# Optimization experiments

Hardware: AMD Instinct MI355X
Metric: run time of the kernel (lower is better)

Reference implementation:

```python
import jax, jax.numpy as jnp
import numpy as np

B = 16384
INPUT_DIM = 256
NUM_SLOTS = 32
SLOT_DIM = 64
NUM_KNOWN = 9
HIDDEN = 128
ITERS = 3
LN_EPS = 1e-5


def _lin(k, fan_in, w_shape, b_shape):
    # torch nn.Linear default init: U(-1/sqrt(fan_in), 1/sqrt(fan_in))
    bound = 1.0 / np.sqrt(fan_in)
    k1, k2 = jax.random.split(k)
    W = jax.random.uniform(k1, w_shape, jnp.float32, -bound, bound)
    b = jax.random.uniform(k2, b_shape, jnp.float32, -bound, bound)
    return W, b


def setup_inputs() -> dict:
    key = jax.random.key(0)
    ks = jax.random.split(key, 20)
    inp = {}
    inp['world_state'] = jax.random.normal(ks[0], (B, INPUT_DIM), jnp.float32)
    inp['eps'] = jax.random.normal(ks[1], (B, NUM_SLOTS, SLOT_DIM), jnp.float32)
    inp['slots_mu'] = jax.random.normal(ks[2], (1, NUM_SLOTS, SLOT_DIM), jnp.float32)
    inp['slots_sigma'] = jnp.ones((1, NUM_SLOTS, SLOT_DIM), jnp.float32) * 0.1
    inp['Wi'], inp['bi'] = _lin(ks[3], INPUT_DIM, (INPUT_DIM, SLOT_DIM), (SLOT_DIM,))
    inp['Wk'], inp['bk'] = _lin(ks[4], SLOT_DIM, (SLOT_DIM, SLOT_DIM), (SLOT_DIM,))
    inp['Wq'], inp['bq'] = _lin(ks[5], SLOT_DIM, (SLOT_DIM, SLOT_DIM), (SLOT_DIM,))
    inp['Wv'], inp['bv'] = _lin(ks[6], SLOT_DIM, (SLOT_DIM, SLOT_DIM), (SLOT_DIM,))
    inp['W_ih'], inp['b_ih'] = _lin(ks[7], SLOT_DIM, (SLOT_DIM, 3 * SLOT_DIM), (3 * SLOT_DIM,))
    inp['W_hh'], inp['b_hh'] = _lin(ks[8], SLOT_DIM, (SLOT_DIM, 3 * SLOT_DIM), (3 * SLOT_DIM,))
    inp['W1'], inp['b1'] = _lin(ks[9], SLOT_DIM, (SLOT_DIM, HIDDEN), (HIDDEN,))
    inp['W2'], inp['b2'] = _lin(ks[10], HIDDEN, (HIDDEN, SLOT_DIM), (SLOT_DIM,))
    inp['g_in'] = jnp.ones((SLOT_DIM,), jnp.float32)
    inp['b_in'] = jnp.zeros((SLOT_DIM,), jnp.float32)
    inp['g_sl'] = jnp.ones((SLOT_DIM,), jnp.float32)
    inp['b_sl'] = jnp.zeros((SLOT_DIM,), jnp.float32)
    inp['g_mlp'] = jnp.ones((SLOT_DIM,), jnp.float32)
    inp['b_mlp'] = jnp.zeros((SLOT_DIM,), jnp.float32)
    inp['Wh1'], inp['bh1'] = _lin(ks[11], SLOT_DIM, (NUM_KNOWN, SLOT_DIM, SLOT_DIM // 2), (NUM_KNOWN, SLOT_DIM // 2))
    inp['Wh2'], inp['bh2'] = _lin(ks[12], SLOT_DIM // 2, (NUM_KNOWN, SLOT_DIM // 2), (NUM_KNOWN,))
    return inp


def _ln(x, g, b):
    mu = jnp.mean(x, axis=-1, keepdims=True)
    var = jnp.mean(jnp.square(x - mu), axis=-1, keepdims=True)
    return (x - mu) / jnp.sqrt(var + LN_EPS) * g + b


def reference(world_state, eps, slots_mu, slots_sigma, Wi, bi, Wk, bk, Wq, bq, Wv, bv,
              W_ih, b_ih, W_hh, b_hh, W1, b1, W2, b2,
              g_in, b_in, g_sl, b_sl, g_mlp, b_mlp, Wh1, bh1, Wh2, bh2):
    scale = SLOT_DIM ** (-0.5)
    x = world_state[:, None, :] @ Wi + bi            # [B,1,D]
    x = _ln(x, g_in, b_in)
    k = x @ Wk + bk                                   # [B,1,D] (loop-invariant)
    v = x @ Wv + bv                                   # [B,1,D]
    slots = slots_mu + slots_sigma * eps              # [B,S,D]
    for _ in range(ITERS):
        prev = slots
        sn = _ln(slots, g_sl, b_sl)
        q = sn @ Wq + bq                              # [B,S,D]
        attn = jnp.einsum('bnd,bsd->bns', k, q) * scale  # [B,1,S]
        attn = jax.nn.softmax(attn, axis=-1) + 1e-8
        attn = attn / jnp.sum(attn, axis=1, keepdims=True)  # dual normalization
        upd = jnp.einsum('bns,bnd->bsd', attn, v)     # [B,S,D]
        # GRUCell
        gi = upd @ W_ih + b_ih                        # [B,S,3D]
        gh = prev @ W_hh + b_hh
        r = jax.nn.sigmoid(gi[..., :SLOT_DIM] + gh[..., :SLOT_DIM])
        z = jax.nn.sigmoid(gi[..., SLOT_DIM:2 * SLOT_DIM] + gh[..., SLOT_DIM:2 * SLOT_DIM])
        n = jnp.tanh(gi[..., 2 * SLOT_DIM:] + r * gh[..., 2 * SLOT_DIM:])
        slots = (1.0 - z) * n + z * prev
        # residual MLP
        h = _ln(slots, g_mlp, b_mlp)
        slots = slots + jax.nn.gelu(h @ W1 + b1, approximate=False) @ W2 + b2
    # known property heads (vectorized over 9 heads)
    s9 = slots[:, :NUM_KNOWN, :]                      # [B,9,D]
    hh = jax.nn.gelu(jnp.einsum('bkd,kdh->bkh', s9, Wh1) + bh1, approximate=False)
    pv = jax.nn.sigmoid(jnp.einsum('bkh,kh->bk', hh, Wh2) + bh2)  # [B,9]
    free_act = jnp.sqrt(jnp.sum(jnp.square(slots[:, NUM_KNOWN:, :]), axis=-1)).mean(axis=0)  # [num_free]
    return (pv, slots, free_act)
```

## Files before the change

kernel.cpp:

```cpp
#include <hip/hip_runtime.h>


typedef __attribute__((ext_vector_type(4))) float f32x4;
typedef __attribute__((ext_vector_type(8))) short s16x8;

#define MFMA16 __builtin_amdgcn_mfma_f32_16x16x32_bf16

#define NB       16384
#define GIB_OFF  (32 + 120*256)
#define PV_N     147456
#define SLOT_N   33554432
#define L2E      1.4426950408889634f

__device__ __forceinline__ unsigned short f2bf(float f){
  unsigned int r;
  asm("v_cvt_pk_bf16_f32 %0, %1, 0" : "=v"(r) : "v"(f));
  return (unsigned short)r;
}
__device__ __forceinline__ float bf2f(unsigned short s){
  unsigned int u = ((unsigned int)s) << 16;
  return __builtin_bit_cast(float, u);
}
__device__ __forceinline__ float sigm(float x){
  return __builtin_amdgcn_rcpf(1.f + __expf(-x));
}
__device__ __forceinline__ float sigm2(float y){
  return __builtin_amdgcn_rcpf(1.f + exp2f(-y));
}
__device__ __forceinline__ float tanh2(float y){
  return 1.f - 2.f*__builtin_amdgcn_rcpf(1.f + exp2f(y));
}
__device__ __forceinline__ float geluf(float x){
  float t = x*x;
  float p = __builtin_fmaf(t, 0.044715f, 1.f);
  float y = (x*2.3022090f)*p;
  return x * __builtin_amdgcn_rcpf(1.f + exp2f(-y));
}

__global__ void prep1_pack(const float* __restrict__ Wi, const float* __restrict__ Wv,
                           const float* __restrict__ Wih, const float* __restrict__ Whh,
                           const float* __restrict__ W1, const float* __restrict__ W2,
                           float* __restrict__ wsf){
  int t = blockIdx.x*256 + threadIdx.x;
  if (blockIdx.x == 0 && threadIdx.x < 32) wsf[threadIdx.x] = 0.f;
  if (t >= 120*64) return;
  int frag = t >> 6, lane = t & 63;
  int q = lane >> 4, idx = lane & 15;
  const float* W; int ncols, ct, kf;
  if      (frag < 24){ W=Whh; ncols=192; ct=frag>>1;      kf=frag&1; }
  else if (frag < 40){ int f=frag-24; W=W1;  ncols=128; ct=f>>1; kf=f&1; }
  else if (frag < 56){ int f=frag-40; W=W2;  ncols=64;  ct=f>>2; kf=f&3; }
  else if (frag < 88){ int f=frag-56; W=Wi;  ncols=64;  ct=f>>3; kf=f&7; }
  else if (frag < 96){ int f=frag-88; W=Wv;  ncols=64;  ct=f>>1; kf=f&1; }
  else               { int f=frag-96; W=Wih; ncols=192; ct=f>>1; kf=f&1; }
  int k0 = kf*32 + q*8;
  int n  = ct*16 + idx;
  float sc = 1.f;
  if (frag < 24) sc = (n < 128) ? L2E : 2.f*L2E;
  unsigned short* dst = (unsigned short*)(wsf + 32) + frag*512 + lane*8;
  #pragma unroll
  for (int j = 0; j < 8; ++j) dst[j] = f2bf(W[(size_t)(k0+j)*ncols + n] * sc);
}

__global__ __launch_bounds__(256) void prep2_gi(
    const float* __restrict__ wstate, const float* __restrict__ bi,
    const float* __restrict__ bv, const float* __restrict__ bih,
    const float* __restrict__ g_in, const float* __restrict__ b_in,
    float* __restrict__ wsf){
  __shared__ __align__(16) unsigned short sxn[4][1152];
  const f32x4 zf = {0.f,0.f,0.f,0.f};
  int tid = threadIdx.x;
  int w = __builtin_amdgcn_readfirstlane(tid >> 6);
  int lane = tid & 63, q = lane >> 4, idx = lane & 15;
  int br0 = blockIdx.x*64 + w*16;
  const unsigned short* fb = (const unsigned short*)(wsf + 32);
  float* gib = wsf + GIB_OFF;

  s16x8 af[8];
  #pragma unroll
  for (int kf = 0; kf < 8; ++kf){
    const float* src = wstate + (size_t)(br0+idx)*256 + kf*32 + q*8;
    f32x4 p0 = *(const f32x4*)(src);
    f32x4 p1 = *(const f32x4*)(src+4);
    s16x8 a;
    a[0]=(short)f2bf(p0[0]); a[1]=(short)f2bf(p0[1]); a[2]=(short)f2bf(p0[2]); a[3]=(short)f2bf(p0[3]);
    a[4]=(short)f2bf(p1[0]); a[5]=(short)f2bf(p1[1]); a[6]=(short)f2bf(p1[2]); a[7]=(short)f2bf(p1[3]);
    af[kf] = a;
  }
  float xv[4][4];
  #pragma unroll
  for (int ct = 0; ct < 4; ++ct){
    f32x4 acc = zf;
    #pragma unroll
    for (int kf = 0; kf < 8; ++kf)
      acc = MFMA16(af[kf], *(const s16x8*)(fb + (56 + ct*8 + kf)*512 + lane*8), acc, 0,0,0);
    float bb = bi[ct*16+idx];
    #pragma unroll
    for (int e = 0; e < 4; ++e) xv[ct][e] = acc[e] + bb;
  }
  #pragma unroll
  for (int e = 0; e < 4; ++e){
    float s1 = xv[0][e]+xv[1][e]+xv[2][e]+xv[3][e];
    float s2 = xv[0][e]*xv[0][e]+xv[1][e]*xv[1][e]+xv[2][e]*xv[2][e]+xv[3][e]*xv[3][e];
    #pragma unroll
    for (int m = 1; m < 16; m <<= 1){ s1 += __shfl_xor(s1,m); s2 += __shfl_xor(s2,m); }
    float mean = s1*(1.f/64.f);
    float var  = s2*(1.f/64.f) - mean*mean;
    float rs   = __builtin_amdgcn_rsqf(var + 1e-5f);
    #pragma unroll
    for (int ct = 0; ct < 4; ++ct){
      int c = ct*16+idx;
      sxn[w][(q*4+e)*72 + c] = f2bf((xv[ct][e]-mean)*rs*g_in[c] + b_in[c]);
    }
  }
  s16x8 xa0 = *(const s16x8*)(&sxn[w][idx*72 + q*8]);
  s16x8 xa1 = *(const s16x8*)(&sxn[w][idx*72 + 32 + q*8]);
  #pragma unroll
  for (int ct = 0; ct < 4; ++ct){
    f32x4 acc = MFMA16(xa0, *(const s16x8*)(fb + (88 + ct*2 + 0)*512 + lane*8), zf, 0,0,0);
    acc       = MFMA16(xa1, *(const s16x8*)(fb + (88 + ct*2 + 1)*512 + lane*8), acc, 0,0,0);
    float bb = bv[ct*16+idx];
    #pragma unroll
    for (int e = 0; e < 4; ++e) sxn[w][(q*4+e)*72 + ct*16+idx] = f2bf(acc[e] + bb);
  }
  s16x8 va0 = *(const s16x8*)(&sxn[w][idx*72 + q*8]);
  s16x8 va1 = *(const s16x8*)(&sxn[w][idx*72 + 32 + q*8]);
  #pragma unroll
  for (int ct = 0; ct < 12; ++ct){
    f32x4 acc = MFMA16(va0, *(const s16x8*)(fb + (96 + ct*2 + 0)*512 + lane*8), zf, 0,0,0);
    acc       = MFMA16(va1, *(const s16x8*)(fb + (96 + ct*2 + 1)*512 + lane*8), acc, 0,0,0);
    float bb = bih[ct*16+idx];
    float sc = (ct < 8) ? L2E : 2.f*L2E;
    #pragma unroll
    for (int e = 0; e < 4; ++e)
      gib[(size_t)(br0 + q*4 + e)*192 + ct*16 + idx] = (acc[e] + bb) * sc;
  }
}

__global__ __launch_bounds__(512, 4) void bank_main(
    const float* __restrict__ eps, const float* __restrict__ smu, const float* __restrict__ ssig,
    const float* __restrict__ bhh, const float* __restrict__ b1v, const float* __restrict__ b2v,
    const float* __restrict__ g_mlp, const float* __restrict__ b_mlp,
    const float* __restrict__ Wh1, const float* __restrict__ bh1,
    const float* __restrict__ Wh2, const float* __restrict__ bh2,
    float* __restrict__ wsf, float* __restrict__ out){
  __shared__ __align__(16) unsigned short swgt[20480];
  __shared__ __align__(16) unsigned short sbuf[8][2176];
  __shared__ float sgi[4][192];
  __shared__ float sbias[512];
  __shared__ float sfree[4][24];
  const f32x4 zf = {0.f,0.f,0.f,0.f};
  int tid = threadIdx.x;
  int w = __builtin_amdgcn_readfirstlane(tid >> 6);
  int lane = tid & 63, q = lane >> 4, idx = lane & 15;
  int pair = w >> 1, half = w & 1;
  int b = blockIdx.x*4 + pair;
  const unsigned short* fb = (const unsigned short*)(wsf + 32);
  const float* gib = wsf + GIB_OFF;

  {
    const uint4* src = (const uint4*)fb;
    uint4* dst = (uint4*)swgt;
    #pragma unroll
    for (int i = 0; i < 5; ++i) dst[tid + 512*i] = src[tid + 512*i];
  }
  {
    int i = tid;
    float vv;
    if      (i < 192) vv = bhh[i] * ((i < 128) ? L2E : 2.f*L2E);
    else if (i < 320) vv = b1v[i-192];
    else if (i < 384) vv = b2v[i-320];
    else if (i < 448) vv = g_mlp[i-384];
    else              vv = b_mlp[i-448];
    sbias[i] = vv;
  }
  if (half == 0){
    #pragma unroll
    for (int jj = 0; jj < 3; ++jj) sgi[pair][jj*64+lane] = gib[(size_t)b*192 + jj*64 + lane];
  }
  unsigned short* S = &sbuf[w][0];
  int s0 = half*16;
  #pragma unroll
  for (int rr = 0; rr < 16; ++rr){
    int s = s0 + rr;
    float ev = eps[((size_t)b*32 + s)*64 + lane];
    S[rr*136 + lane] = f2bf(smu[s*64+lane] + ssig[s*64+lane]*ev);
  }
  __syncthreads();

  size_t obase = (size_t)PV_N + ((size_t)b*32 + s0)*64;
  #pragma unroll 1
  for (int it = 0; it < 3; ++it){
    s16x8 a0 = *(const s16x8*)(&S[idx*136 + q*8]);
    s16x8 a1 = *(const s16x8*)(&S[idx*136 + 32 + q*8]);
    f32x4 gacc[12];
    #pragma unroll
    for (int ct = 0; ct < 12; ++ct){
      f32x4 acc = MFMA16(a0, *(const s16x8*)(&swgt[(ct*2+0)*512 + lane*8]), zf, 0,0,0);
      gacc[ct]  = MFMA16(a1, *(const s16x8*)(&swgt[(ct*2+1)*512 + lane*8]), acc, 0,0,0);
    }
    float nsv[4][4];
    #pragma unroll
    for (int ct = 0; ct < 4; ++ct){
      int c = ct*16+idx;
      float cr = sgi[pair][c]     + sbias[c];
      float cz = sgi[pair][64+c]  + sbias[64+c];
      float cn = sgi[pair][128+c];
      float bn = sbias[128+c];
      #pragma unroll
      for (int e = 0; e < 4; ++e){
        float r = sigm2(cr + gacc[ct][e]);
        float z = sigm2(cz + gacc[4+ct][e]);
        float n = tanh2(cn + r*(gacc[8+ct][e] + bn));
        float prev = bf2f(S[(q*4+e)*136 + c]);
        nsv[ct][e] = (1.f - z)*n + z*prev;
      }
    }
    #pragma unroll
    for (int e = 0; e < 4; ++e){
      float s1 = nsv[0][e]+nsv[1][e]+nsv[2][e]+nsv[3][e];
      float s2 = nsv[0][e]*nsv[0][e]+nsv[1][e]*nsv[1][e]+nsv[2][e]*nsv[2][e]+nsv[3][e]*nsv[3][e];
      #pragma unroll
      for (int m = 1; m < 16; m <<= 1){ s1 += __shfl_xor(s1,m); s2 += __shfl_xor(s2,m); }
      float mean = s1*(1.f/64.f);
      float var  = s2*(1.f/64.f) - mean*mean;
      float rs   = __builtin_amdgcn_rsqf(var + 1e-5f);
      #pragma unroll
      for (int ct = 0; ct < 4; ++ct){
        int c = ct*16+idx;
        S[(q*4+e)*136 + c] = f2bf((nsv[ct][e]-mean)*rs*sbias[384+c] + sbias[448+c]);
      }
    }
    s16x8 h0 = *(const s16x8*)(&S[idx*136 + q*8]);
    s16x8 h1 = *(const s16x8*)(&S[idx*136 + 32 + q*8]);
    f32x4 macc[8];
    #pragma unroll
    for (int ct = 0; ct < 8; ++ct){
      f32x4 acc = MFMA16(h0, *(const s16x8*)(&swgt[(24+ct*2+0)*512 + lane*8]), zf, 0,0,0);
      macc[ct]  = MFMA16(h1, *(const s16x8*)(&swgt[(24+ct*2+1)*512 + lane*8]), acc, 0,0,0);
    }
    #pragma unroll
    for (int ct = 0; ct < 8; ++ct){
      int c = ct*16+idx;
      float bb = sbias[192+c];
      #pragma unroll
      for (int e = 0; e < 4; ++e)
        S[(q*4+e)*136 + c] = f2bf(geluf(macc[ct][e] + bb));
    }
    s16x8 t0 = *(const s16x8*)(&S[idx*136 +       q*8]);
    s16x8 t1 = *(const s16x8*)(&S[idx*136 + 32  + q*8]);
    s16x8 t2 = *(const s16x8*)(&S[idx*136 + 64  + q*8]);
    s16x8 t3 = *(const s16x8*)(&S[idx*136 + 96  + q*8]);
    #pragma unroll
    for (int ct = 0; ct < 4; ++ct){
      f32x4 acc = MFMA16(t0, *(const s16x8*)(fb + (40+ct*4+0)*512 + lane*8), zf, 0,0,0);
      acc       = MFMA16(t1, *(const s16x8*)(fb + (40+ct*4+1)*512 + lane*8), acc, 0,0,0);
      acc       = MFMA16(t2, *(const s16x8*)(fb + (40+ct*4+2)*512 + lane*8), acc, 0,0,0);
      acc       = MFMA16(t3, *(const s16x8*)(fb + (40+ct*4+3)*512 + lane*8), acc, 0,0,0);
      int c = ct*16+idx;
      float bb = sbias[320+c];
      #pragma unroll
      for (int e = 0; e < 4; ++e){
        float val = nsv[ct][e] + acc[e] + bb;
        S[(q*4+e)*136 + c] = f2bf(val);
        if (it == 2) out[obase + (size_t)(q*4+e)*64 + c] = val;
      }
    }
  }
  __syncthreads();

  if (half == 0){
    int hh = lane & 31, h2 = lane >> 5;
    #pragma unroll 1
    for (int kb = 0; kb < 5; ++kb){
      int k = kb*2 + h2;
      if (k < 9){
        const float* wp = Wh1 + (size_t)k*2048 + hh;
        float a0=0.f, a1=0.f, a2=0.f, a3=0.f;
        #pragma unroll 4
        for (int dd = 0; dd < 64; dd += 4){
          a0 += bf2f(S[k*136 + dd  ]) * wp[(dd  )*32];
          a1 += bf2f(S[k*136 + dd+1]) * wp[(dd+1)*32];
          a2 += bf2f(S[k*136 + dd+2]) * wp[(dd+2)*32];
          a3 += bf2f(S[k*136 + dd+3]) * wp[(dd+3)*32];
        }
        float a = bh1[k*32 + hh] + (a0 + a1) + (a2 + a3);
        float u = geluf(a);
        float p = u * Wh2[k*32 + hh];
        #pragma unroll
        for (int m = 1; m < 32; m <<= 1) p += __shfl_xor(p, m);
        p = sigm(p + bh2[k]);
        if (hh == 0) out[(size_t)b*9 + k] = p;
      }
    }
  } else {
    const unsigned short* SL = &sbuf[w-1][0];
    #pragma unroll 1
    for (int s = 9; s < 32; ++s){
      const unsigned short* src = (s < 16) ? (SL + s*136) : (S + (s-16)*136);
      float v = bf2f(src[lane]);
      float sq = v*v;
      #pragma unroll
      for (int m = 1; m < 64; m <<= 1) sq += __shfl_xor(sq, m);
      if (lane == 0) sfree[pair][s-9] = sqrtf(sq);
    }
  }
  __syncthreads();
  if (tid < 23) atomicAdd(&wsf[tid], sfree[0][tid] + sfree[1][tid] + sfree[2][tid] + sfree[3][tid]);
}

__global__ void bank_final(const float* __restrict__ wsf, float* __restrict__ out){
  int t = threadIdx.x;
  if (t < 23) out[(size_t)PV_N + SLOT_N + t] = wsf[t] * (1.f/16384.f);
}

extern "C" void kernel_launch(void* const* d_in, const int* in_sizes, int n_in,
                              void* d_out, int out_size, void* d_ws, size_t ws_size,
                              hipStream_t stream){
  (void)in_sizes; (void)n_in; (void)out_size; (void)ws_size;
  const float* wstate = (const float*)d_in[0];
  const float* eps    = (const float*)d_in[1];
  const float* smu    = (const float*)d_in[2];
  const float* ssig   = (const float*)d_in[3];
  const float* Wi     = (const float*)d_in[4];
  const float* bi     = (const float*)d_in[5];
  const float* Wv     = (const float*)d_in[10];
  const float* bv     = (const float*)d_in[11];
  const float* Wih    = (const float*)d_in[12];
  const float* bih    = (const float*)d_in[13];
  const float* Whh    = (const float*)d_in[14];
  const float* bhh    = (const float*)d_in[15];
  const float* W1     = (const float*)d_in[16];
  const float* b1     = (const float*)d_in[17];
  const float* W2     = (const float*)d_in[18];
  const float* b2     = (const float*)d_in[19];
  const float* g_in   = (const float*)d_in[20];
  const float* b_in   = (const float*)d_in[21];
  const float* g_mlp  = (const float*)d_in[24];
  const float* b_mlp  = (const float*)d_in[25];
  const float* Wh1    = (const float*)d_in[26];
  const float* bh1    = (const float*)d_in[27];
  const float* Wh2    = (const float*)d_in[28];
  const float* bh2    = (const float*)d_in[29];
  float* out = (float*)d_out;
  float* wsf = (float*)d_ws;

  prep1_pack<<<dim3(30),   dim3(256), 0, stream>>>(Wi, Wv, Wih, Whh, W1, W2, wsf);
  prep2_gi  <<<dim3(256),  dim3(256), 0, stream>>>(wstate, bi, bv, bih, g_in, b_in, wsf);
  bank_main <<<dim3(4096), dim3(512), 0, stream>>>(eps, smu, ssig, bhh, b1, b2,
                                                   g_mlp, b_mlp, Wh1, bh1, Wh2, bh2,
                                                   wsf, out);
  bank_final<<<dim3(1),    dim3(64),  0, stream>>>(wsf, out);
}
```

Baseline: 637.0 us.

## Fuse input projection into main kernel and read weights from global/L1

```diff
diff --git a/kernel.cpp b/kernel.cpp
--- a/kernel.cpp
+++ b/kernel.cpp
@@ -7,15 +7,14 @@
 #define MFMA16 __builtin_amdgcn_mfma_f32_16x16x32_bf16
 
 #define NB       16384
-#define GIB_OFF  (32 + 120*256)
 #define PV_N     147456
 #define SLOT_N   33554432
 #define L2E      1.4426950408889634f
 
 __device__ __forceinline__ unsigned short f2bf(float f){
-  unsigned int r;
-  asm("v_cvt_pk_bf16_f32 %0, %1, 0" : "=v"(r) : "v"(f));
-  return (unsigned short)r;
+  unsigned int u = __builtin_bit_cast(unsigned int, f);
+  u += 0x7fffu + ((u >> 16) & 1u);
+  return (unsigned short)(u >> 16);
 }
 __device__ __forceinline__ float bf2f(unsigned short s){
   unsigned int u = ((unsigned int)s) << 16;
@@ -62,90 +61,18 @@
   for (int j = 0; j < 8; ++j) dst[j] = f2bf(W[(size_t)(k0+j)*ncols + n] * sc);
 }
 
-__global__ __launch_bounds__(256) void prep2_gi(
-    const float* __restrict__ wstate, const float* __restrict__ bi,
-    const float* __restrict__ bv, const float* __restrict__ bih,
+__global__ __launch_bounds__(512, 6) void bank_main(
+    const float* __restrict__ wstate,
+    const float* __restrict__ eps, const float* __restrict__ smu, const float* __restrict__ ssig,
+    const float* __restrict__ bi, const float* __restrict__ bv, const float* __restrict__ bih,
     const float* __restrict__ g_in, const float* __restrict__ b_in,
-    float* __restrict__ wsf){
-  __shared__ __align__(16) unsigned short sxn[4][1152];
-  const f32x4 zf = {0.f,0.f,0.f,0.f};
-  int tid = threadIdx.x;
-  int w = __builtin_amdgcn_readfirstlane(tid >> 6);
-  int lane = tid & 63, q = lane >> 4, idx = lane & 15;
-  int br0 = blockIdx.x*64 + w*16;
-  const unsigned short* fb = (const unsigned short*)(wsf + 32);
-  float* gib = wsf + GIB_OFF;
-
-  s16x8 af[8];
-  #pragma unroll
-  for (int kf = 0; kf < 8; ++kf){
-    const float* src = wstate + (size_t)(br0+idx)*256 + kf*32 + q*8;
-    f32x4 p0 = *(const f32x4*)(src);
-    f32x4 p1 = *(const f32x4*)(src+4);
-    s16x8 a;
-    a[0]=(short)f2bf(p0[0]); a[1]=(short)f2bf(p0[1]); a[2]=(short)f2bf(p0[2]); a[3]=(short)f2bf(p0[3]);
-    a[4]=(short)f2bf(p1[0]); a[5]=(short)f2bf(p1[1]); a[6]=(short)f2bf(p1[2]); a[7]=(short)f2bf(p1[3]);
-    af[kf] = a;
-  }
-  float xv[4][4];
-  #pragma unroll
-  for (int ct = 0; ct < 4; ++ct){
-    f32x4 acc = zf;
-    #pragma unroll
-    for (int kf = 0; kf < 8; ++kf)
-      acc = MFMA16(af[kf], *(const s16x8*)(fb + (56 + ct*8 + kf)*512 + lane*8), acc, 0,0,0);
-    float bb = bi[ct*16+idx];
-    #pragma unroll
-    for (int e = 0; e < 4; ++e) xv[ct][e] = acc[e] + bb;
-  }
-  #pragma unroll
-  for (int e = 0; e < 4; ++e){
-    float s1 = xv[0][e]+xv[1][e]+xv[2][e]+xv[3][e];
-    float s2 = xv[0][e]*xv[0][e]+xv[1][e]*xv[1][e]+xv[2][e]*xv[2][e]+xv[3][e]*xv[3][e];
-    #pragma unroll
-    for (int m = 1; m < 16; m <<= 1){ s1 += __shfl_xor(s1,m); s2 += __shfl_xor(s2,m); }
-    float mean = s1*(1.f/64.f);
-    float var  = s2*(1.f/64.f) - mean*mean;
-    float rs   = __builtin_amdgcn_rsqf(var + 1e-5f);
-    #pragma unroll
-    for (int ct = 0; ct < 4; ++ct){
-      int c = ct*16+idx;
-      sxn[w][(q*4+e)*72 + c] = f2bf((xv[ct][e]-mean)*rs*g_in[c] + b_in[c]);
-    }
-  }
-  s16x8 xa0 = *(const s16x8*)(&sxn[w][idx*72 + q*8]);
-  s16x8 xa1 = *(const s16x8*)(&sxn[w][idx*72 + 32 + q*8]);
-  #pragma unroll
-  for (int ct = 0; ct < 4; ++ct){
-    f32x4 acc = MFMA16(xa0, *(const s16x8*)(fb + (88 + ct*2 + 0)*512 + lane*8), zf, 0,0,0);
-    acc       = MFMA16(xa1, *(const s16x8*)(fb + (88 + ct*2 + 1)*512 + lane*8), acc, 0,0,0);
-    float bb = bv[ct*16+idx];
-    #pragma unroll
-    for (int e = 0; e < 4; ++e) sxn[w][(q*4+e)*72 + ct*16+idx] = f2bf(acc[e] + bb);
-  }
-  s16x8 va0 = *(const s16x8*)(&sxn[w][idx*72 + q*8]);
-  s16x8 va1 = *(const s16x8*)(&sxn[w][idx*72 + 32 + q*8]);
-  #pragma unroll
-  for (int ct = 0; ct < 12; ++ct){
-    f32x4 acc = MFMA16(va0, *(const s16x8*)(fb + (96 + ct*2 + 0)*512 + lane*8), zf, 0,0,0);
-    acc       = MFMA16(va1, *(const s16x8*)(fb + (96 + ct*2 + 1)*512 + lane*8), acc, 0,0,0);
-    float bb = bih[ct*16+idx];
-    float sc = (ct < 8) ? L2E : 2.f*L2E;
-    #pragma unroll
-    for (int e = 0; e < 4; ++e)
-      gib[(size_t)(br0 + q*4 + e)*192 + ct*16 + idx] = (acc[e] + bb) * sc;
-  }
-}
-
-__global__ __launch_bounds__(512, 4) void bank_main(
-    const float* __restrict__ eps, const float* __restrict__ smu, const float* __restrict__ ssig,
     const float* __restrict__ bhh, const float* __restrict__ b1v, const float* __restrict__ b2v,
     const float* __restrict__ g_mlp, const float* __restrict__ b_mlp,
     const float* __restrict__ Wh1, const float* __restrict__ bh1,
     const float* __restrict__ Wh2, const float* __restrict__ bh2,
     float* __restrict__ wsf, float* __restrict__ out){
-  __shared__ __align__(16) unsigned short swgt[20480];
   __shared__ __align__(16) unsigned short sbuf[8][2176];
+  __shared__ __align__(16) unsigned short sxn[1152];
   __shared__ float sgi[4][192];
   __shared__ float sbias[512];
   __shared__ float sfree[4][24];
@@ -156,14 +83,7 @@
   int pair = w >> 1, half = w & 1;
   int b = blockIdx.x*4 + pair;
   const unsigned short* fb = (const unsigned short*)(wsf + 32);
-  const float* gib = wsf + GIB_OFF;
-
-  {
-    const uint4* src = (const uint4*)fb;
-    uint4* dst = (uint4*)swgt;
-    #pragma unroll
-    for (int i = 0; i < 5; ++i) dst[tid + 512*i] = src[tid + 512*i];
-  }
+
   {
     int i = tid;
     float vv;
@@ -174,10 +94,6 @@
     else              vv = b_mlp[i-448];
     sbias[i] = vv;
   }
-  if (half == 0){
-    #pragma unroll
-    for (int jj = 0; jj < 3; ++jj) sgi[pair][jj*64+lane] = gib[(size_t)b*192 + jj*64 + lane];
-  }
   unsigned short* S = &sbuf[w][0];
   int s0 = half*16;
   #pragma unroll
@@ -186,6 +102,70 @@
     float ev = eps[((size_t)b*32 + s)*64 + lane];
     S[rr*136 + lane] = f2bf(smu[s*64+lane] + ssig[s*64+lane]*ev);
   }
+
+  if (w == 0){
+    int brow = (idx < 4) ? idx : 3;
+    const float* srcb = wstate + (size_t)(blockIdx.x*4 + brow)*256;
+    s16x8 af[8];
+    #pragma unroll
+    for (int kf = 0; kf < 8; ++kf){
+      f32x4 p0 = *(const f32x4*)(srcb + kf*32 + q*8);
+      f32x4 p1 = *(const f32x4*)(srcb + kf*32 + q*8 + 4);
+      s16x8 a;
+      a[0]=(short)f2bf(p0[0]); a[1]=(short)f2bf(p0[1]); a[2]=(short)f2bf(p0[2]); a[3]=(short)f2bf(p0[3]);
+      a[4]=(short)f2bf(p1[0]); a[5]=(short)f2bf(p1[1]); a[6]=(short)f2bf(p1[2]); a[7]=(short)f2bf(p1[3]);
+      af[kf] = a;
+    }
+    float xv[4][4];
+    #pragma unroll
+    for (int ct = 0; ct < 4; ++ct){
+      f32x4 acc = zf;
+      #pragma unroll
+      for (int kf = 0; kf < 8; ++kf)
+        acc = MFMA16(af[kf], *(const s16x8*)(fb + (56 + ct*8 + kf)*512 + lane*8), acc, 0,0,0);
+      float bb = bi[ct*16+idx];
+      #pragma unroll
+      for (int e = 0; e < 4; ++e) xv[ct][e] = acc[e] + bb;
+    }
+    #pragma unroll
+    for (int e = 0; e < 4; ++e){
+      float s1 = xv[0][e]+xv[1][e]+xv[2][e]+xv[3][e];
+      float s2 = xv[0][e]*xv[0][e]+xv[1][e]*xv[1][e]+xv[2][e]*xv[2][e]+xv[3][e]*xv[3][e];
+      #pragma unroll
+      for (int m = 1; m < 16; m <<= 1){ s1 += __shfl_xor(s1,m); s2 += __shfl_xor(s2,m); }
+      float mean = s1*(1.f/64.f);
+      float var  = s2*(1.f/64.f) - mean*mean;
+      float rs   = __builtin_amdgcn_rsqf(var + 1e-5f);
+      #pragma unroll
+      for (int ct = 0; ct < 4; ++ct){
+        int c = ct*16+idx;
+        sxn[(q*4+e)*72 + c] = f2bf((xv[ct][e]-mean)*rs*g_in[c] + b_in[c]);
+      }
+    }
+    s16x8 xa0 = *(const s16x8*)(&sxn[idx*72 + q*8]);
+    s16x8 xa1 = *(const s16x8*)(&sxn[idx*72 + 32 + q*8]);
+    #pragma unroll
+    for (int ct = 0; ct < 4; ++ct){
+      f32x4 acc = MFMA16(xa0, *(const s16x8*)(fb + (88 + ct*2 + 0)*512 + lane*8), zf, 0,0,0);
+      acc       = MFMA16(xa1, *(const s16x8*)(fb + (88 + ct*2 + 1)*512 + lane*8), acc, 0,0,0);
+      float bb = bv[ct*16+idx];
+      #pragma unroll
+      for (int e = 0; e < 4; ++e) sxn[(q*4+e)*72 + ct*16+idx] = f2bf(acc[e] + bb);
+    }
+    s16x8 va0 = *(const s16x8*)(&sxn[idx*72 + q*8]);
+    s16x8 va1 = *(const s16x8*)(&sxn[idx*72 + 32 + q*8]);
+    #pragma unroll
+    for (int ct = 0; ct < 12; ++ct){
+      f32x4 acc = MFMA16(va0, *(const s16x8*)(fb + (96 + ct*2 + 0)*512 + lane*8), zf, 0,0,0);
+      acc       = MFMA16(va1, *(const s16x8*)(fb + (96 + ct*2 + 1)*512 + lane*8), acc, 0,0,0);
+      float bb = bih[ct*16+idx];
+      float sc = (ct < 8) ? L2E : 2.f*L2E;
+      if (q == 0){
+        #pragma unroll
+        for (int e = 0; e < 4; ++e) sgi[e][ct*16+idx] = (acc[e] + bb) * sc;
+      }
+    }
+  }
   __syncthreads();
 
   size_t obase = (size_t)PV_N + ((size_t)b*32 + s0)*64;
@@ -193,15 +173,15 @@
   for (int it = 0; it < 3; ++it){
     s16x8 a0 = *(const s16x8*)(&S[idx*136 + q*8]);
     s16x8 a1 = *(const s16x8*)(&S[idx*136 + 32 + q*8]);
-    f32x4 gacc[12];
-    #pragma unroll
-    for (int ct = 0; ct < 12; ++ct){
-      f32x4 acc = MFMA16(a0, *(const s16x8*)(&swgt[(ct*2+0)*512 + lane*8]), zf, 0,0,0);
-      gacc[ct]  = MFMA16(a1, *(const s16x8*)(&swgt[(ct*2+1)*512 + lane*8]), acc, 0,0,0);
-    }
     float nsv[4][4];
     #pragma unroll
     for (int ct = 0; ct < 4; ++ct){
+      f32x4 gr = MFMA16(a0, *(const s16x8*)(fb + ((   ct)*2+0)*512 + lane*8), zf, 0,0,0);
+      gr       = MFMA16(a1, *(const s16x8*)(fb + ((   ct)*2+1)*512 + lane*8), gr, 0,0,0);
+      f32x4 gz = MFMA16(a0, *(const s16x8*)(fb + ((4+ ct)*2+0)*512 + lane*8), zf, 0,0,0);
+      gz       = MFMA16(a1, *(const s16x8*)(fb + ((4+ ct)*2+1)*512 + lane*8), gz, 0,0,0);
+      f32x4 gn = MFMA16(a0, *(const s16x8*)(fb + ((8+ ct)*2+0)*512 + lane*8), zf, 0,0,0);
+      gn       = MFMA16(a1, *(const s16x8*)(fb + ((8+ ct)*2+1)*512 + lane*8), gn, 0,0,0);
       int c = ct*16+idx;
       float cr = sgi[pair][c]     + sbias[c];
       float cz = sgi[pair][64+c]  + sbias[64+c];
@@ -209,9 +189,9 @@
       float bn = sbias[128+c];
       #pragma unroll
       for (int e = 0; e < 4; ++e){
-        float r = sigm2(cr + gacc[ct][e]);
-        float z = sigm2(cz + gacc[4+ct][e]);
-        float n = tanh2(cn + r*(gacc[8+ct][e] + bn));
+        float r = sigm2(cr + gr[e]);
+        float z = sigm2(cz + gz[e]);
+        float n = tanh2(cn + r*(gn[e] + bn));
         float prev = bf2f(S[(q*4+e)*136 + c]);
         nsv[ct][e] = (1.f - z)*n + z*prev;
       }
@@ -233,19 +213,15 @@
     }
     s16x8 h0 = *(const s16x8*)(&S[idx*136 + q*8]);
     s16x8 h1 = *(const s16x8*)(&S[idx*136 + 32 + q*8]);
-    f32x4 macc[8];
     #pragma unroll
     for (int ct = 0; ct < 8; ++ct){
-      f32x4 acc = MFMA16(h0, *(const s16x8*)(&swgt[(24+ct*2+0)*512 + lane*8]), zf, 0,0,0);
-      macc[ct]  = MFMA16(h1, *(const s16x8*)(&swgt[(24+ct*2+1)*512 + lane*8]), acc, 0,0,0);
-    }
-    #pragma unroll
-    for (int ct = 0; ct < 8; ++ct){
+      f32x4 acc = MFMA16(h0, *(const s16x8*)(fb + (24+ct*2+0)*512 + lane*8), zf, 0,0,0);
+      acc       = MFMA16(h1, *(const s16x8*)(fb + (24+ct*2+1)*512 + lane*8), acc, 0,0,0);
       int c = ct*16+idx;
       float bb = sbias[192+c];
       #pragma unroll
       for (int e = 0; e < 4; ++e)
-        S[(q*4+e)*136 + c] = f2bf(geluf(macc[ct][e] + bb));
+        S[(q*4+e)*136 + c] = f2bf(geluf(acc[e] + bb));
     }
     s16x8 t0 = *(const s16x8*)(&S[idx*136 +       q*8]);
     s16x8 t1 = *(const s16x8*)(&S[idx*136 + 32  + q*8]);
@@ -346,9 +322,10 @@
   float* wsf = (float*)d_ws;
 
   prep1_pack<<<dim3(30),   dim3(256), 0, stream>>>(Wi, Wv, Wih, Whh, W1, W2, wsf);
-  prep2_gi  <<<dim3(256),  dim3(256), 0, stream>>>(wstate, bi, bv, bih, g_in, b_in, wsf);
-  bank_main <<<dim3(4096), dim3(512), 0, stream>>>(eps, smu, ssig, bhh, b1, b2,
-                                                   g_mlp, b_mlp, Wh1, bh1, Wh2, bh2,
+  bank_main <<<dim3(4096), dim3(512), 0, stream>>>(wstate, eps, smu, ssig,
+                                                   bi, bv, bih, g_in, b_in,
+                                                   bhh, b1, b2, g_mlp, b_mlp,
+                                                   Wh1, bh1, Wh2, bh2,
                                                    wsf, out);
   bank_final<<<dim3(1),    dim3(64),  0, stream>>>(wsf, out);
 }
```

Measured after the change: 1.187 ms. 86.4% more time.
